# Kernel optimization log

Hardware: AMD Instinct MI355X
Metric: run time of the kernel (lower is better)

## Reference

```python
import jax, jax.numpy as jnp
import numpy as np

EPS = 1e-8  # torch.cosine_similarity default eps


def setup_inputs() -> dict:
    key = jax.random.key(0)
    ks = jax.random.split(key, 6)
    B, S, H, D = 512, 4096, 32, 16
    return {
        "decoder_hidden_final_layer": jax.random.normal(ks[0], (B, H), dtype=jnp.float32),
        "encoder_outputs": jax.random.normal(ks[1], (B, S, H), dtype=jnp.float32),
        "Wq": jax.random.normal(ks[2], (D, H), dtype=jnp.float32) * 0.1,
        "bq": jax.random.normal(ks[3], (D,), dtype=jnp.float32) * 0.1,
        "Wk": jax.random.normal(ks[4], (D, H), dtype=jnp.float32) * 0.1,
        "bk": jax.random.normal(ks[5], (D,), dtype=jnp.float32) * 0.1,
    }


def reference(decoder_hidden_final_layer, encoder_outputs, Wq, bq, Wk, bk):
    # q projection of encoder outputs: [B,S,D]; k projection of decoder state: [B,D]
    q = jnp.einsum("bsh,dh->bsd", encoder_outputs, Wq) + bq
    k = decoder_hidden_final_layer @ Wk.T + bk
    # cosine similarity: normalize once, then a single contraction (same math as
    # torch.cosine_similarity with eps clamp on the norms)
    qn = q / jnp.maximum(jnp.linalg.norm(q, axis=-1, keepdims=True), EPS)
    kn = k / jnp.maximum(jnp.linalg.norm(k, axis=-1, keepdims=True), EPS)
    attention = jnp.einsum("bsd,bd->bs", qn, kn)  # [B,S]
    weightings = jax.nn.log_softmax(attention, axis=1)  # softmax over S (torch dim=1)
    return weightings[:, None, :]  # transpose(1,2): [B,1,S]
```

## Files before the change

kernel.cpp:

```cpp
#include <hip/hip_runtime.h>
#include <math.h>

#define BB    512
#define SS    4096
#define HH    32
#define DD    16
#define NT    256
#define WAVES 4
#define RPW   (SS / WAVES)
#define TPW   (RPW / 16)
#define DEPTH 4
#define NGRP  (TPW / DEPTH)
#define EPSI  1e-8f

typedef __attribute__((ext_vector_type(8))) short   short8;
typedef __attribute__((ext_vector_type(4))) float   floatx4;

__device__ __forceinline__ short bf16_of(float f) {
    union { float f; unsigned u; } v; v.f = f;
    return (short)((v.u + 0x7FFFu + ((v.u >> 16) & 1u)) >> 16);
}

template <int CTRL>
__device__ __forceinline__ float dpp_add(float x) {
    int xi = __builtin_bit_cast(int, x);
    int yi = __builtin_amdgcn_update_dpp(0, xi, CTRL, 0xF, 0xF, true);
    return x + __builtin_bit_cast(float, yi);
}
__device__ __forceinline__ float red16(float x) {
    x = dpp_add<0xB1>(x);
    x = dpp_add<0x4E>(x);
    x = dpp_add<0x141>(x);
    x = dpp_add<0x140>(x);
    return x;
}

__global__ __launch_bounds__(NT, 2)
void attn_cos_logsoftmax(const float* __restrict__ dec,
                         const float* __restrict__ enc,
                         const float* __restrict__ Wq,
                         const float* __restrict__ bq,
                         const float* __restrict__ Wk,
                         const float* __restrict__ bk,
                         float* __restrict__ out)
{
    __shared__ float attS[SS];
    __shared__ float redM[WAVES], redS[WAVES];

    const int t    = threadIdx.x;
    const int b    = blockIdx.x;
    const int lane = t & 63;
    const int wv   = t >> 6;
    const int l15  = lane & 15;
    const int quad = lane >> 4;

    const float* encb = enc + (size_t)b * SS * HH;
    const int rowbase = wv * RPW;

    const float* src0 = encb + (size_t)(rowbase + l15) * HH + quad * 8;

    float4 pf[DEPTH][2];
#pragma unroll
    for (int s = 0; s < DEPTH; ++s) {
        const float* p = src0 + (size_t)s * 16 * HH;
        pf[s][0] = *(const float4*)p;
        pf[s][1] = *(const float4*)(p + 4);
    }

    short8 bfrag;
    {
        const float* wp = Wq + l15 * HH + quad * 8;
        float4 w0 = *(const float4*)wp;
        float4 w1 = *(const float4*)(wp + 4);
        bfrag[0] = bf16_of(w0.x); bfrag[1] = bf16_of(w0.y);
        bfrag[2] = bf16_of(w0.z); bfrag[3] = bf16_of(w0.w);
        bfrag[4] = bf16_of(w1.x); bfrag[5] = bf16_of(w1.y);
        bfrag[6] = bf16_of(w1.z); bfrag[7] = bf16_of(w1.w);
    }
    const float bqV = bq[l15];

    float knV;
    {
        float a = bk[l15];
        const float* wk = Wk + l15 * HH;
#pragma unroll
        for (int h = 0; h < HH; ++h) a = fmaf(wk[h], dec[b * HH + h], a);
        float ssk = red16(a * a);
        knV = a * (1.f / fmaxf(sqrtf(ssk), EPSI));
    }

    float* attW = attS + rowbase;
    for (int g = 0; g < NGRP; ++g) {
#pragma unroll
        for (int s = 0; s < DEPTH; ++s) {
            const int i = g * DEPTH + s;
            float4 p0 = pf[s][0];
            float4 p1 = pf[s][1];
            if (g + 1 < NGRP) {
                const float* p = src0 + (size_t)(i + DEPTH) * 16 * HH;
                pf[s][0] = *(const float4*)p;
                pf[s][1] = *(const float4*)(p + 4);
            }
            short8 afrag;
            afrag[0] = bf16_of(p0.x); afrag[1] = bf16_of(p0.y);
            afrag[2] = bf16_of(p0.z); afrag[3] = bf16_of(p0.w);
            afrag[4] = bf16_of(p1.x); afrag[5] = bf16_of(p1.y);
            afrag[6] = bf16_of(p1.z); afrag[7] = bf16_of(p1.w);

            floatx4 acc = {0.f, 0.f, 0.f, 0.f};
            acc = __builtin_amdgcn_mfma_f32_16x16x32_bf16(afrag, bfrag, acc, 0, 0, 0);

            float4 av; float* avp = &av.x;
#pragma unroll
            for (int r = 0; r < 4; ++r) {
                float qv = acc[r] + bqV;
                float ss = red16(qv * qv);
                float nu = red16(qv * knV);
                avp[r] = nu / fmaxf(sqrtf(ss), EPSI);
            }
            if (l15 == 0)
                *(float4*)&attW[i * 16 + quad * 4] = av;
        }
    }
    __syncthreads();

    float m = -INFINITY;
#pragma unroll
    for (int i = 0; i < 16; ++i) m = fmaxf(m, attS[t + i * NT]);
#pragma unroll
    for (int off = 32; off >= 1; off >>= 1) m = fmaxf(m, __shfl_down(m, off));
    if (lane == 0) redM[wv] = m;
    __syncthreads();
    const float M = fmaxf(fmaxf(redM[0], redM[1]), fmaxf(redM[2], redM[3]));

    float s = 0.f;
#pragma unroll
    for (int i = 0; i < 16; ++i) s += __expf(attS[t + i * NT] - M);
#pragma unroll
    for (int off = 32; off >= 1; off >>= 1) s += __shfl_down(s, off);
    if (lane == 0) redS[wv] = s;
    __syncthreads();
    const float S = (redS[0] + redS[1]) + (redS[2] + redS[3]);
    const float logZ = M + __logf(S);

    float4* ob4 = (float4*)(out + (size_t)b * SS);
#pragma unroll
    for (int i = 0; i < 4; ++i) {
        float4 a4 = *(const float4*)&attS[(t + i * NT) * 4];
        a4.x -= logZ; a4.y -= logZ; a4.z -= logZ; a4.w -= logZ;
        ob4[t + i * NT] = a4;
    }
}

extern "C" void kernel_launch(void* const* d_in, const int* in_sizes, int n_in,
                              void* d_out, int out_size, void* d_ws, size_t ws_size,
                              hipStream_t stream) {
    const float* dec = (const float*)d_in[0];
    const float* enc = (const float*)d_in[1];
    const float* Wq  = (const float*)d_in[2];
    const float* bq  = (const float*)d_in[3];
    const float* Wk  = (const float*)d_in[4];
    const float* bk  = (const float*)d_in[5];
    float* out = (float*)d_out;

    attn_cos_logsoftmax<<<dim3(BB), dim3(NT), 0, stream>>>(dec, enc, Wq, bq, Wk, bk, out);
}
```

Before: 375.4 us.

## Double waves per block, use hardware bf16 convert, transpose MFMA to cut reductions

Raises the block to 512 threads (8 waves) with a min-blocks hint of 4, giving more in-flight loads per CU. It replaces the software bf16 rounding with packed v_cvt_pk_bf16_f32 instructions and swaps the MFMA operands so each lane holds 4 projection dimensions of one row. The per-row norm and dot product then need only two cross-quad bpermute adds instead of eight 16-lane DPP reductions per row. Bias is folded into the accumulator init and the division is replaced by rsq, which slightly changes rounding.

```diff
diff --git a/kernel.cpp b/kernel.cpp
--- a/kernel.cpp
+++ b/kernel.cpp
@@ -5,8 +5,8 @@
 #define SS    4096
 #define HH    32
 #define DD    16
-#define NT    256
-#define WAVES 4
+#define NT    512
+#define WAVES 8
 #define RPW   (SS / WAVES)
 #define TPW   (RPW / 16)
 #define DEPTH 4
@@ -15,11 +15,6 @@
 
 typedef __attribute__((ext_vector_type(8))) short   short8;
 typedef __attribute__((ext_vector_type(4))) float   floatx4;
-
-__device__ __forceinline__ short bf16_of(float f) {
-    union { float f; unsigned u; } v; v.f = f;
-    return (short)((v.u + 0x7FFFu + ((v.u >> 16) & 1u)) >> 16);
-}
 
 template <int CTRL>
 __device__ __forceinline__ float dpp_add(float x) {
@@ -35,7 +30,24 @@
     return x;
 }
 
-__global__ __launch_bounds__(NT, 2)
+__device__ __forceinline__ short8 cvt_bf16x8(float4 a, float4 b) {
+    unsigned p0, p1, p2, p3;
+    asm("v_cvt_pk_bf16_f32 %0, %1, %2" : "=&v"(p0) : "v"(a.x), "v"(a.y));
+    asm("v_cvt_pk_bf16_f32 %0, %1, %2" : "=&v"(p1) : "v"(a.z), "v"(a.w));
+    asm("v_cvt_pk_bf16_f32 %0, %1, %2" : "=&v"(p2) : "v"(b.x), "v"(b.y));
+    asm("v_cvt_pk_bf16_f32 %0, %1, %2" : "=&v"(p3) : "v"(b.z), "v"(b.w));
+    union { unsigned u[4]; short8 s; } r;
+    r.u[0] = p0; r.u[1] = p1; r.u[2] = p2; r.u[3] = p3;
+    return r.s;
+}
+
+__device__ __forceinline__ float bperm_add(int addr, float x) {
+    int xi = __builtin_bit_cast(int, x);
+    int yi = __builtin_amdgcn_ds_bpermute(addr, xi);
+    return x + __builtin_bit_cast(float, yi);
+}
+
+__global__ __launch_bounds__(NT, 4)
 void attn_cos_logsoftmax(const float* __restrict__ dec,
                          const float* __restrict__ enc,
                          const float* __restrict__ Wq,
@@ -67,27 +79,27 @@
         pf[s][1] = *(const float4*)(p + 4);
     }
 
-    short8 bfrag;
-    {
-        const float* wp = Wq + l15 * HH + quad * 8;
-        float4 w0 = *(const float4*)wp;
-        float4 w1 = *(const float4*)(wp + 4);
-        bfrag[0] = bf16_of(w0.x); bfrag[1] = bf16_of(w0.y);
-        bfrag[2] = bf16_of(w0.z); bfrag[3] = bf16_of(w0.w);
-        bfrag[4] = bf16_of(w1.x); bfrag[5] = bf16_of(w1.y);
-        bfrag[6] = bf16_of(w1.z); bfrag[7] = bf16_of(w1.w);
-    }
-    const float bqV = bq[l15];
+    const float* wp = Wq + l15 * HH + quad * 8;
+    const short8 wfrag = cvt_bf16x8(*(const float4*)wp, *(const float4*)(wp + 4));
 
-    float knV;
+    const float4 bq4 = *(const float4*)(bq + quad * 4);
+
+    float knr0, knr1, knr2, knr3;
     {
         float a = bk[l15];
         const float* wk = Wk + l15 * HH;
 #pragma unroll
         for (int h = 0; h < HH; ++h) a = fmaf(wk[h], dec[b * HH + h], a);
         float ssk = red16(a * a);
-        knV = a * (1.f / fmaxf(sqrtf(ssk), EPSI));
+        float knV = a * (1.f / fmaxf(sqrtf(ssk), EPSI));
+        knr0 = __shfl(knV, 4 * quad + 0);
+        knr1 = __shfl(knV, 4 * quad + 1);
+        knr2 = __shfl(knV, 4 * quad + 2);
+        knr3 = __shfl(knV, 4 * quad + 3);
     }
+
+    const int bp16 = (lane ^ 16) << 2;
+    const int bp32 = (lane ^ 32) << 2;
 
     float* attW = attS + rowbase;
     for (int g = 0; g < NGRP; ++g) {
@@ -101,51 +113,56 @@
                 pf[s][0] = *(const float4*)p;
                 pf[s][1] = *(const float4*)(p + 4);
             }
-            short8 afrag;
-            afrag[0] = bf16_of(p0.x); afrag[1] = bf16_of(p0.y);
-            afrag[2] = bf16_of(p0.z); afrag[3] = bf16_of(p0.w);
-            afrag[4] = bf16_of(p1.x); afrag[5] = bf16_of(p1.y);
-            afrag[6] = bf16_of(p1.z); afrag[7] = bf16_of(p1.w);
+            short8 efrag = cvt_bf16x8(p0, p1);
 
-            floatx4 acc = {0.f, 0.f, 0.f, 0.f};
-            acc = __builtin_amdgcn_mfma_f32_16x16x32_bf16(afrag, bfrag, acc, 0, 0, 0);
+            floatx4 acc = {bq4.x, bq4.y, bq4.z, bq4.w};
+            acc = __builtin_amdgcn_mfma_f32_16x16x32_bf16(wfrag, efrag, acc, 0, 0, 0);
 
-            float4 av; float* avp = &av.x;
-#pragma unroll
-            for (int r = 0; r < 4; ++r) {
-                float qv = acc[r] + bqV;
-                float ss = red16(qv * qv);
-                float nu = red16(qv * knV);
-                avp[r] = nu / fmaxf(sqrtf(ss), EPSI);
-            }
-            if (l15 == 0)
-                *(float4*)&attW[i * 16 + quad * 4] = av;
+            float ss = 0.f, nu = 0.f;
+            float qv;
+            qv = acc[0]; ss = fmaf(qv, qv, ss); nu = fmaf(qv, knr0, nu);
+            qv = acc[1]; ss = fmaf(qv, qv, ss); nu = fmaf(qv, knr1, nu);
+            qv = acc[2]; ss = fmaf(qv, qv, ss); nu = fmaf(qv, knr2, nu);
+            qv = acc[3]; ss = fmaf(qv, qv, ss); nu = fmaf(qv, knr3, nu);
+
+            ss = bperm_add(bp16, ss);
+            nu = bperm_add(bp16, nu);
+            ss = bperm_add(bp32, ss);
+            nu = bperm_add(bp32, nu);
+
+            float ssc = fmaxf(ss, EPSI * EPSI);
+            float att = nu * __builtin_amdgcn_rsqf(ssc);
+            if (lane < 16) attW[i * 16 + lane] = att;
         }
     }
     __syncthreads();
 
     float m = -INFINITY;
 #pragma unroll
-    for (int i = 0; i < 16; ++i) m = fmaxf(m, attS[t + i * NT]);
+    for (int i = 0; i < SS / NT; ++i) m = fmaxf(m, attS[t + i * NT]);
 #pragma unroll
     for (int off = 32; off >= 1; off >>= 1) m = fmaxf(m, __shfl_down(m, off));
     if (lane == 0) redM[wv] = m;
     __syncthreads();
-    const float M = fmaxf(fmaxf(redM[0], redM[1]), fmaxf(redM[2], redM[3]));
+    float M = redM[0];
+#pragma unroll
+    for (int w = 1; w < WAVES; ++w) M = fmaxf(M, redM[w]);
 
-    float s = 0.f;
+    float sacc = 0.f;
 #pragma unroll
-    for (int i = 0; i < 16; ++i) s += __expf(attS[t + i * NT] - M);
+    for (int i = 0; i < SS / NT; ++i) sacc += __expf(attS[t + i * NT] - M);
 #pragma unroll
-    for (int off = 32; off >= 1; off >>= 1) s += __shfl_down(s, off);
-    if (lane == 0) redS[wv] = s;
+    for (int off = 32; off >= 1; off >>= 1) sacc += __shfl_down(sacc, off);
+    if (lane == 0) redS[wv] = sacc;
     __syncthreads();
-    const float S = (redS[0] + redS[1]) + (redS[2] + redS[3]);
+    float S = 0.f;
+#pragma unroll
+    for (int w = 0; w < WAVES; ++w) S += redS[w];
     const float logZ = M + __logf(S);
 
     float4* ob4 = (float4*)(out + (size_t)b * SS);
 #pragma unroll
-    for (int i = 0; i < 4; ++i) {
+    for (int i = 0; i < SS / NT / 4; ++i) {
         float4 a4 = *(const float4*)&attS[(t + i * NT) * 4];
         a4.x -= logZ; a4.y -= logZ; a4.z -= logZ; a4.w -= logZ;
         ob4[t + i * NT] = a4;
```

Result: faster. 366.7 us (-2.3%).
